# Optimization experiments

Hardware: AMD Instinct MI355X
Metric: run time of the kernel (lower is better)

The kernel has to match this reference:

```python
import jax, jax.numpy as jnp
from jax import lax
import numpy as np

DN = ('NCHW', 'OIHW', 'NCHW')
PAD = [(1, 1), (1, 1)]  # padding=1 each side
STRIDE = (1, 1)


def setup_inputs() -> dict:
    key = jax.random.key(0)
    k0, k1, k2, k3, k4, k5 = jax.random.split(key, 6)
    B, Cin, Cout, H, W, K, FES = 32, 96, 144, 56, 56, 3, 3
    fan_main = Cin * K * K
    fan_extra = FES * K * K
    x = jax.random.normal(k0, (B, Cin, H, W), dtype=jnp.float32)
    extra_inputs = jax.random.normal(k1, (B, Cout * FES), dtype=jnp.float32)
    Wm = jax.random.normal(k2, (Cout, Cin, K, K), dtype=jnp.float32) / np.sqrt(fan_main)
    bm = jax.random.normal(k3, (Cout,), dtype=jnp.float32) * 0.01
    Wx = jax.random.normal(k4, (Cout, FES, K, K), dtype=jnp.float32) / np.sqrt(fan_extra)
    bx = jax.random.normal(k5, (Cout,), dtype=jnp.float32) * 0.01
    return {"x": x, "extra_inputs": extra_inputs, "Wm": Wm, "bm": bm, "Wx": Wx, "bx": bx}


def reference(x, extra_inputs, Wm, bm, Wx, bx):
    # main path: standard conv + bias
    main = lax.conv_general_dilated(x, Wm, STRIDE, PAD, dimension_numbers=DN)
    main = main + bm[None, :, None, None]

    B = x.shape[0]
    Cout, FES, kh, kw = Wx.shape
    H2, W2 = main.shape[2], main.shape[3]

    # Extra path: each extra conv operates on a spatially-constant map, so
    # conv(const_c) = const_c * conv(ones). Compute per-(out,fes)-kernel response
    # to a ones map once (captures zero-padding boundary effects exactly),
    # then combine via a batched einsum — collapsing the per-channel loop.
    ones = jnp.ones((1, 1, x.shape[2], x.shape[3]), dtype=x.dtype)
    M = lax.conv_general_dilated(
        ones, Wx.reshape(Cout * FES, 1, kh, kw), STRIDE, PAD, dimension_numbers=DN
    )  # [1, Cout*FES, H2, W2]
    M = M.reshape(Cout, FES, H2, W2)

    extra = extra_inputs.reshape(B, Cout, FES)
    extra_out = jnp.einsum('bif,ifhw->bihw', extra, M) + bx[None, :, None, None]

    return main + extra_out
```

## Files before the change

### kernel.cpp

```cpp
#include <hip/hip_runtime.h>
#include <hip/hip_bf16.h>

#define B_    32
#define CIN   96
#define COUT  144
#define H_    56
#define W_    56
#define HW    3136
#define NPIX  100352
#define KTOT  864
#define MT    256
#define TAPSZ (COUT*CIN)

typedef short  short8  __attribute__((ext_vector_type(8)));
typedef float  floatx4 __attribute__((ext_vector_type(4)));

__device__ __attribute__((aligned(64))) float g_zero[64];

__device__ __forceinline__ unsigned short f2bf(float f) {
    union { float f; unsigned int u; } v; v.f = f;
    unsigned int u = v.u;
    return (unsigned short)((u + 0x7FFFu + ((u >> 16) & 1u)) >> 16);
}

__device__ __forceinline__ void glds16(const void* g, void* l) {
    __builtin_amdgcn_global_load_lds(
        (const __attribute__((address_space(1))) unsigned int*)g,
        (__attribute__((address_space(3))) unsigned int*)l, 16, 0, 0);
}

#define TB 1568
#define WB 486
__global__ __launch_bounds__(256) void prep_all(const float* __restrict__ x,
                                                unsigned short* __restrict__ xT,
                                                const float* __restrict__ Wm,
                                                unsigned short* __restrict__ Wt,
                                                const float* __restrict__ extra,
                                                const float* __restrict__ Wx,
                                                const float* __restrict__ bm,
                                                const float* __restrict__ bx,
                                                float* __restrict__ E) {
    __shared__ __align__(16) unsigned short tile[64][CIN + 8];
    int blk = blockIdx.x;
    int t = threadIdx.x;
    if (blk < TB) {
        int b   = blk / 49;
        int hw0 = (blk % 49) * 64;
        const float* xb = x + (size_t)b * CIN * HW;
        for (int i = t; i < CIN * 16; i += 256) {
            int ci = i >> 4, seg = i & 15;
            float4 v = *(const float4*)(xb + (size_t)ci * HW + hw0 + seg * 4);
            int hwl = seg * 4;
            tile[hwl + 0][ci] = f2bf(v.x);
            tile[hwl + 1][ci] = f2bf(v.y);
            tile[hwl + 2][ci] = f2bf(v.z);
            tile[hwl + 3][ci] = f2bf(v.w);
        }
        __syncthreads();
        int row = t >> 2, part = t & 3;
        const uint4* s = (const uint4*)&tile[row][part * 24];
        uint4* d = (uint4*)(xT + ((size_t)b * HW + hw0 + row) * CIN + part * 24);
        d[0] = s[0]; d[1] = s[1]; d[2] = s[2];
    } else if (blk < TB + WB) {
        int i = (blk - TB) * 256 + t;
        int tap = i / TAPSZ;
        int rem = i - tap * TAPSZ;
        int co  = rem / CIN, ci = rem - co * CIN;
        Wt[i] = f2bf(Wm[((size_t)co * CIN + ci) * 9 + tap]);
    } else {
        int i = (blk - TB - WB) * 256 + t;
        int b = i / COUT, co = i - b * COUT;
        float base = bm[co] + bx[co];
        float m[3][3] = {{0,0,0},{0,0,0},{0,0,0}};
        for (int f = 0; f < 3; ++f) {
            float e = extra[(size_t)b * (COUT * 3) + co * 3 + f];
            const float* w = Wx + ((size_t)co * 3 + f) * 9;
            for (int rc = 0; rc < 3; ++rc) {
                int kh0 = (rc == 0) ? 1 : 0;
                int kh1 = (rc == 2) ? 1 : 2;
                for (int cc = 0; cc < 3; ++cc) {
                    int kw0 = (cc == 0) ? 1 : 0;
                    int kw1 = (cc == 2) ? 1 : 2;
                    float s = 0.f;
                    for (int kh = kh0; kh <= kh1; ++kh)
                        for (int kw = kw0; kw <= kw1; ++kw)
                            s += w[kh * 3 + kw];
                    m[rc][cc] += e * s;
                }
            }
        }
        float* dst = E + (size_t)i * 9;
        for (int rc = 0; rc < 3; ++rc)
            for (int cc = 0; cc < 3; ++cc)
                dst[rc * 3 + cc] = base + m[rc][cc];
    }
}

__global__ __launch_bounds__(256, 1) void conv_gemm(const unsigned short* __restrict__ xT,
                                                    const unsigned short* __restrict__ Wt,
                                                    const float* __restrict__ E,
                                                    float* __restrict__ out) {
    __shared__ __align__(16) unsigned short Bs[2 * TAPSZ];

    int tid = threadIdx.x;
    int wv = tid >> 6, lane = tid & 63;
    int r16 = lane & 15, q = lane >> 4;
    int pixBase = blockIdx.x * MT;

    floatx4 acc[4][9];
    #pragma unroll
    for (int m = 0; m < 4; ++m)
        #pragma unroll
        for (int n = 0; n < 9; ++n)
            acc[m][n] = (floatx4){0.f, 0.f, 0.f, 0.f};

    int aIdx[4], hA[4], wA[4];
    #pragma unroll
    for (int ms = 0; ms < 4; ++ms) {
        int p = pixBase + wv * 64 + ms * 16 + r16;
        aIdx[ms] = p * CIN;
        int hw = p % HW;
        hA[ms] = hw / W_;
        wA[ms] = hw - hA[ms] * W_;
    }
    const unsigned short* gz = (const unsigned short*)g_zero;

    int bSrc[7];
    #pragma unroll
    for (int j = 0; j < 7; ++j) {
        int s = tid + j * 256;
        int g = s / COUT, co = s - g * COUT;
        bSrc[j] = co * CIN + g * 8;
    }
    const bool bTail = (tid < 192);

    const unsigned short* BpBase = Bs + (q * COUT + r16) * 8;

    short8 a[2][4][3];

    {
        const unsigned short* wsrc = Wt;
        #pragma unroll
        for (int j = 0; j < 6; ++j)
            glds16(wsrc + bSrc[j], (void*)(Bs + tid * 8 + j * 2048));
        if (bTail)
            glds16(wsrc + bSrc[6], (void*)(Bs + tid * 8 + 6 * 2048));
        const int dh = -1, dw = -1, off = (dh * W_ + dw) * CIN;
        #pragma unroll
        for (int ms = 0; ms < 4; ++ms) {
            bool valid = ((unsigned)(hA[ms] + dh) < H_) && ((unsigned)(wA[ms] + dw) < W_);
            const unsigned short* base = valid ? (xT + aIdx[ms] + off) : gz;
            #pragma unroll
            for (int ks = 0; ks < 3; ++ks)
                a[0][ms][ks] = *(const short8*)(base + ks * 32 + q * 8);
        }
    }
    __syncthreads();

    #pragma unroll
    for (int tap = 0; tap < 9; ++tap) {
        const int cur = tap & 1, nxt = cur ^ 1;

        if (tap < 8) {
            const int tap2 = tap + 1;
            const int dh2 = tap2 / 3 - 1, dw2 = tap2 - (tap2 / 3) * 3 - 1;
            const unsigned short* wsrc = Wt + tap2 * TAPSZ;
            unsigned short* bd = Bs + nxt * TAPSZ;
            #pragma unroll
            for (int j = 0; j < 6; ++j)
                glds16(wsrc + bSrc[j], (void*)(bd + tid * 8 + j * 2048));
            if (bTail)
                glds16(wsrc + bSrc[6], (void*)(bd + tid * 8 + 6 * 2048));
            const int off2 = (dh2 * W_ + dw2) * CIN;
            #pragma unroll
            for (int ms = 0; ms < 4; ++ms) {
                bool valid = ((unsigned)(hA[ms] + dh2) < H_) && ((unsigned)(wA[ms] + dw2) < W_);
                const unsigned short* base = valid ? (xT + aIdx[ms] + off2) : gz;
                #pragma unroll
                for (int ks = 0; ks < 3; ++ks)
                    a[nxt][ms][ks] = *(const short8*)(base + ks * 32 + q * 8);
            }
        }

        const unsigned short* Bp = BpBase + cur * TAPSZ;
        #pragma unroll
        for (int ks = 0; ks < 3; ++ks) {
            short8 bf[9];
            #pragma unroll
            for (int n = 0; n < 9; ++n)
                bf[n] = *(const short8*)(Bp + ks * 4608 + n * 128);
            #pragma unroll
            for (int n = 0; n < 9; ++n)
                #pragma unroll
                for (int ms = 0; ms < 4; ++ms)
                    acc[ms][n] = __builtin_amdgcn_mfma_f32_16x16x32_bf16(
                        a[cur][ms][ks], bf[n], acc[ms][n], 0, 0, 0);
        }

        __syncthreads();
    }

    #pragma unroll
    for (int ms = 0; ms < 4; ++ms) {
        int p0 = pixBase + wv * 64 + ms * 16 + q * 4;
        int b  = p0 / HW;
        int hw0 = p0 - b * HW;
        int h = hw0 / W_;
        int w0 = hw0 - h * W_;
        int rc = (h == 0) ? 0 : ((h == H_ - 1) ? 2 : 1);
        int cc0 = (w0 == 0) ? 0 : ((w0 == W_ - 1) ? 2 : 1);
        int cc1 = (w0 + 1 == W_ - 1) ? 2 : 1;
        int cc2 = (w0 + 2 == W_ - 1) ? 2 : 1;
        int cc3 = (w0 + 3 == W_ - 1) ? 2 : 1;
        const float* Ebase = E + (size_t)b * COUT * 9 + rc * 3;
        float* outB = out + (size_t)b * COUT * HW + hw0;
        #pragma unroll
        for (int n = 0; n < 9; ++n) {
            int co = n * 16 + r16;
            const float* Eb = Ebase + co * 9;
            float4 v;
            v.x = acc[ms][n][0] + Eb[cc0];
            v.y = acc[ms][n][1] + Eb[cc1];
            v.z = acc[ms][n][2] + Eb[cc2];
            v.w = acc[ms][n][3] + Eb[cc3];
            *(float4*)(outB + (size_t)co * HW) = v;
        }
    }
}

extern "C" void kernel_launch(void* const* d_in, const int* in_sizes, int n_in,
                              void* d_out, int out_size, void* d_ws, size_t ws_size,
                              hipStream_t stream) {
    const float* x     = (const float*)d_in[0];
    const float* extra = (const float*)d_in[1];
    const float* Wm    = (const float*)d_in[2];
    const float* bm    = (const float*)d_in[3];
    const float* Wx    = (const float*)d_in[4];
    const float* bx    = (const float*)d_in[5];
    float* out = (float*)d_out;

    const size_t XT_BYTES = (size_t)NPIX * CIN * 2;
    const size_t WT_BYTES = (size_t)COUT * KTOT * 2;
    const size_t E_BYTES  = (size_t)B_ * COUT * 9 * 4;
    if (ws_size < XT_BYTES + WT_BYTES + E_BYTES) return;

    unsigned short* xT = (unsigned short*)d_ws;
    unsigned short* Wt = (unsigned short*)((char*)d_ws + XT_BYTES);
    float*          E  = (float*)((char*)d_ws + XT_BYTES + WT_BYTES);

    prep_all<<<TB + WB + 18, 256, 0, stream>>>(x, xT, Wm, Wt, extra, Wx, bm, bx, E);
    conv_gemm<<<NPIX / MT, 256, 0, stream>>>(xT, Wt, E, out);
}
```

Before: 159.6 us.

## Cut register pressure for two blocks per CU and pre-swizzle weight layout

The conv GEMM kernel now targets two workgroups per CU by raising launch bounds. To make that fit, it drops the double-buffered A register fragments and instead reloads each A slice right after its MFMAs consume it. It also loads B fragments three at a time rather than nine, and no longer unrolls the tap loop. The weight prep kernel writes Wt in an [tap][group8][co][8] order, so the LDS fill becomes a plain contiguous copy with no per-thread source index array. The risk is exposed global load latency on A, because prefetch now overlaps less with compute within one block.

```diff
diff --git a/kernel.cpp b/kernel.cpp
--- a/kernel.cpp
+++ b/kernel.cpp
@@ -63,9 +63,13 @@
         d[0] = s[0]; d[1] = s[1]; d[2] = s[2];
     } else if (blk < TB + WB) {
         int i = (blk - TB) * 256 + t;
-        int tap = i / TAPSZ;
-        int rem = i - tap * TAPSZ;
-        int co  = rem / CIN, ci = rem - co * CIN;
+        int tap = i / 13824;
+        int r1  = i - tap * 13824;
+        int g   = r1 / 1152;
+        int r2  = r1 - g * 1152;
+        int co  = r2 >> 3;
+        int e   = r2 & 7;
+        int ci  = g * 8 + e;
         Wt[i] = f2bf(Wm[((size_t)co * CIN + ci) * 9 + tap]);
     } else {
         int i = (blk - TB - WB) * 256 + t;
@@ -96,7 +100,7 @@
     }
 }
 
-__global__ __launch_bounds__(256, 1) void conv_gemm(const unsigned short* __restrict__ xT,
+__global__ __launch_bounds__(256, 2) void conv_gemm(const unsigned short* __restrict__ xT,
                                                     const unsigned short* __restrict__ Wt,
                                                     const float* __restrict__ E,
                                                     float* __restrict__ out) {
@@ -125,26 +129,19 @@
     }
     const unsigned short* gz = (const unsigned short*)g_zero;
 
-    int bSrc[7];
-    #pragma unroll
-    for (int j = 0; j < 7; ++j) {
-        int s = tid + j * 256;
-        int g = s / COUT, co = s - g * COUT;
-        bSrc[j] = co * CIN + g * 8;
-    }
     const bool bTail = (tid < 192);
 
     const unsigned short* BpBase = Bs + (q * COUT + r16) * 8;
 
-    short8 a[2][4][3];
+    short8 a[4][3];
 
     {
         const unsigned short* wsrc = Wt;
         #pragma unroll
         for (int j = 0; j < 6; ++j)
-            glds16(wsrc + bSrc[j], (void*)(Bs + tid * 8 + j * 2048));
+            glds16(wsrc + tid * 8 + j * 2048, (void*)(Bs + tid * 8 + j * 2048));
         if (bTail)
-            glds16(wsrc + bSrc[6], (void*)(Bs + tid * 8 + 6 * 2048));
+            glds16(wsrc + tid * 8 + 6 * 2048, (void*)(Bs + tid * 8 + 6 * 2048));
         const int dh = -1, dw = -1, off = (dh * W_ + dw) * CIN;
         #pragma unroll
         for (int ms = 0; ms < 4; ++ms) {
@@ -152,49 +149,64 @@
             const unsigned short* base = valid ? (xT + aIdx[ms] + off) : gz;
             #pragma unroll
             for (int ks = 0; ks < 3; ++ks)
-                a[0][ms][ks] = *(const short8*)(base + ks * 32 + q * 8);
+                a[ms][ks] = *(const short8*)(base + ks * 32 + q * 8);
         }
     }
     __syncthreads();
 
-    #pragma unroll
+    #pragma unroll 1
     for (int tap = 0; tap < 9; ++tap) {
         const int cur = tap & 1, nxt = cur ^ 1;
-
-        if (tap < 8) {
+        const bool pf = (tap < 8);
+
+        const unsigned short* aBase[4];
+        if (pf) {
             const int tap2 = tap + 1;
-            const int dh2 = tap2 / 3 - 1, dw2 = tap2 - (tap2 / 3) * 3 - 1;
+            const int r3   = tap2 / 3;
+            const int dh2  = r3 - 1, dw2 = tap2 - r3 * 3 - 1;
             const unsigned short* wsrc = Wt + tap2 * TAPSZ;
             unsigned short* bd = Bs + nxt * TAPSZ;
             #pragma unroll
             for (int j = 0; j < 6; ++j)
-                glds16(wsrc + bSrc[j], (void*)(bd + tid * 8 + j * 2048));
+                glds16(wsrc + tid * 8 + j * 2048, (void*)(bd + tid * 8 + j * 2048));
             if (bTail)
-                glds16(wsrc + bSrc[6], (void*)(bd + tid * 8 + 6 * 2048));
+                glds16(wsrc + tid * 8 + 6 * 2048, (void*)(bd + tid * 8 + 6 * 2048));
             const int off2 = (dh2 * W_ + dw2) * CIN;
             #pragma unroll
             for (int ms = 0; ms < 4; ++ms) {
                 bool valid = ((unsigned)(hA[ms] + dh2) < H_) && ((unsigned)(wA[ms] + dw2) < W_);
-                const unsigned short* base = valid ? (xT + aIdx[ms] + off2) : gz;
-                #pragma unroll
-                for (int ks = 0; ks < 3; ++ks)
-                    a[nxt][ms][ks] = *(const short8*)(base + ks * 32 + q * 8);
+                aBase[ms] = valid ? (xT + aIdx[ms] + off2) : gz;
             }
+        } else {
+            #pragma unroll
+            for (int ms = 0; ms < 4; ++ms)
+                aBase[ms] = gz;
         }
 
         const unsigned short* Bp = BpBase + cur * TAPSZ;
         #pragma unroll
         for (int ks = 0; ks < 3; ++ks) {
-            short8 bf[9];
-            #pragma unroll
-            for (int n = 0; n < 9; ++n)
-                bf[n] = *(const short8*)(Bp + ks * 4608 + n * 128);
-            #pragma unroll
-            for (int n = 0; n < 9; ++n)
+            #pragma unroll
+            for (int n3 = 0; n3 < 3; ++n3) {
+                short8 b0 = *(const short8*)(Bp + ks * 4608 + (n3 * 3 + 0) * 128);
+                short8 b1 = *(const short8*)(Bp + ks * 4608 + (n3 * 3 + 1) * 128);
+                short8 b2 = *(const short8*)(Bp + ks * 4608 + (n3 * 3 + 2) * 128);
                 #pragma unroll
                 for (int ms = 0; ms < 4; ++ms)
-                    acc[ms][n] = __builtin_amdgcn_mfma_f32_16x16x32_bf16(
-                        a[cur][ms][ks], bf[n], acc[ms][n], 0, 0, 0);
+                    acc[ms][n3 * 3 + 0] = __builtin_amdgcn_mfma_f32_16x16x32_bf16(
+                        a[ms][ks], b0, acc[ms][n3 * 3 + 0], 0, 0, 0);
+                #pragma unroll
+                for (int ms = 0; ms < 4; ++ms)
+                    acc[ms][n3 * 3 + 1] = __builtin_amdgcn_mfma_f32_16x16x32_bf16(
+                        a[ms][ks], b1, acc[ms][n3 * 3 + 1], 0, 0, 0);
+                #pragma unroll
+                for (int ms = 0; ms < 4; ++ms)
+                    acc[ms][n3 * 3 + 2] = __builtin_amdgcn_mfma_f32_16x16x32_bf16(
+                        a[ms][ks], b2, acc[ms][n3 * 3 + 2], 0, 0, 0);
+            }
+            #pragma unroll
+            for (int ms = 0; ms < 4; ++ms)
+                a[ms][ks] = *(const short8*)(aBase[ms] + ks * 32 + q * 8);
         }
 
         __syncthreads();
```

New measurement: 148.8 us. -6.7%, faster.
